# Kernel tuning notes

Hardware: AMD Instinct MI355X
Metric: run time of the kernel (lower is better)

Reference implementation:

```python
import jax, jax.numpy as jnp
import numpy as np

# dims: G groups, A authors/group, P posts/author, DIN token-pooled feat, DEMB sentence-BERT dim
G, A, P, DIN, DEMB, HP, HA = 16, 64, 32, 768, 384, 256, 128


def setup_inputs() -> dict:
    key = jax.random.key(0)
    ks = jax.random.split(key, 8)
    s = lambda k, shape, scale: (jax.random.normal(k, shape, jnp.float32) * scale)
    return {
        "x": jax.random.normal(ks[0], (G, A, P, DIN), jnp.float32),
        "w_embed": s(ks[1], (DIN, DEMB), 0.02),   # BERT pooled-projection stand-in
        "b_embed": jnp.zeros((DEMB,), jnp.float32),
        "k_post": s(ks[2], (DEMB, 4 * HP), 0.05),  # Keras LSTM kernel, gates [i|f|c|o]
        "r_post": s(ks[3], (HP, 4 * HP), 0.05),    # recurrent kernel
        "b_post": jnp.zeros((4 * HP,), jnp.float32),
        "k_auth": s(ks[4], (HP, 4 * HA), 0.05),
        "r_auth": s(ks[5], (HA, 4 * HA), 0.05),
        "b_auth": jnp.zeros((4 * HA,), jnp.float32),
    }


def _lstm(x, Wk, Wr, b):
    """Keras-style LSTM, returns final hidden state. x: [B,T,D] -> [B,H]."""
    B = x.shape[0]
    H = Wr.shape[0]
    # precompute input projections for all timesteps in one GEMM: [T,B,4H]
    z = jnp.einsum('btd,dh->tbh', x, Wk) + b

    def step(carry, zt):
        h, c = carry
        g = zt + h @ Wr
        i, f, gg, o = jnp.split(g, 4, axis=-1)  # Keras gate order i,f,c,o
        c = jax.nn.sigmoid(f) * c + jax.nn.sigmoid(i) * jnp.tanh(gg)
        h = jax.nn.sigmoid(o) * jnp.tanh(c)
        return (h, c), None

    h0 = jnp.zeros((B, H), x.dtype)
    (h, _), _ = jax.lax.scan(step, (h0, h0), z)
    return h


def reference(x, w_embed, b_embed, k_post, r_post, b_post, k_auth, r_auth, b_auth):
    g, a, p, _ = x.shape
    # sentence embedding per post (BERT stand-in): [G,A,P,DEMB]
    e = jnp.einsum('gapd,de->gape', x, w_embed) + b_embed
    # LSTM over posts, batched across all (group, author) pairs: [G,A,HP]
    h_post = _lstm(e.reshape(g * a, p, e.shape[-1]), k_post, r_post, b_post)
    h_post = h_post.reshape(g, a, -1)
    # LSTM over authors: [G,HA]
    return _lstm(h_post, k_auth, r_auth, b_auth)
```

## Files before the change

kernel.cpp:

```cpp
#include <hip/hip_runtime.h>
#include <cstdint>
#include <cstddef>

#define G_    16
#define A_    64
#define P_    32
#define DIN_  768
#define DEMB_ 384
#define HP_   256
#define HA_   128
#define GA_   1024
#define N1_   1024
#define N2_   512
#define TCH   16

typedef float    f32x4   __attribute__((ext_vector_type(4)));
typedef _Float16 half8_t __attribute__((ext_vector_type(8)));
typedef _Float16 half4_t __attribute__((ext_vector_type(4)));

__device__ __forceinline__ float sigmoidf_(float x) { return 1.0f / (1.0f + __expf(-x)); }
__device__ __forceinline__ float tanhf_(float x) { return 2.0f / (1.0f + __expf(-2.0f * x)) - 1.0f; }
__device__ __forceinline__ _Float16 us2h(unsigned short u) { _Float16 h; __builtin_memcpy(&h, &u, 2); return h; }
__device__ __forceinline__ unsigned short h2us(_Float16 h) { unsigned short u; __builtin_memcpy(&u, &h, 2); return u; }


__global__ __launch_bounds__(256) void k_wk(const float* __restrict__ w_embed,
                                            const float* __restrict__ k_post,
                                            float* __restrict__ Bmat) {
    int j  = blockIdx.x * 256 + threadIdx.x;
    int k0 = blockIdx.y * 4;
    float acc0 = 0.f, acc1 = 0.f, acc2 = 0.f, acc3 = 0.f;
    for (int d = 0; d < DEMB_; ++d) {
        float kp = k_post[(size_t)d * N1_ + j];
        acc0 += w_embed[(size_t)(k0 + 0) * DEMB_ + d] * kp;
        acc1 += w_embed[(size_t)(k0 + 1) * DEMB_ + d] * kp;
        acc2 += w_embed[(size_t)(k0 + 2) * DEMB_ + d] * kp;
        acc3 += w_embed[(size_t)(k0 + 3) * DEMB_ + d] * kp;
    }
    Bmat[(size_t)(k0 + 0) * N1_ + j] = acc0;
    Bmat[(size_t)(k0 + 1) * N1_ + j] = acc1;
    Bmat[(size_t)(k0 + 2) * N1_ + j] = acc2;
    Bmat[(size_t)(k0 + 3) * N1_ + j] = acc3;
}

__global__ __launch_bounds__(256) void k_bias_p(const float* __restrict__ b_embed,
                                                const float* __restrict__ k_post,
                                                const float* __restrict__ b_post,
                                                float* __restrict__ biasZp) {
    int p = blockIdx.x * 256 + threadIdx.x;
    int n = (p >> 6) * 16 + (p & 15) + 256 * ((p >> 4) & 3);
    float acc = b_post[n];
    for (int d = 0; d < DEMB_; ++d)
        acc += b_embed[d] * k_post[(size_t)d * N1_ + n];
    biasZp[p] = acc;
}

__global__ __launch_bounds__(256) void k_t16(const float* __restrict__ Bmat,
                                             _Float16* __restrict__ Bt16) {
    __shared__ float tile[64][65];
    const int tid = threadIdx.x;
    const int p0 = blockIdx.x * 64;
    const int k0 = blockIdx.y * 64;
    const int jgrp = p0 >> 6;
#pragma unroll
    for (int i = 0; i < 16; ++i) {
        int idx = i * 256 + tid;
        int pp = idx & 63, kk = idx >> 6;
        int n = jgrp * 16 + (pp & 15) + 256 * ((pp >> 4) & 3);
        tile[pp][kk] = Bmat[(size_t)(k0 + kk) * N1_ + n];
    }
    __syncthreads();
    const int pp = tid >> 2;
    const int kq = (tid & 3) * 16;
    _Float16 buf[16];
#pragma unroll
    for (int i = 0; i < 16; ++i) buf[i] = (_Float16)tile[pp][kq + i];
    _Float16* dst = &Bt16[(size_t)(p0 + pp) * DIN_ + k0 + kq];
    *(half8_t*)dst       = *(half8_t*)&buf[0];
    *(half8_t*)(dst + 8) = *(half8_t*)&buf[8];
}

__global__ __launch_bounds__(256) void k_bfrag(const float* __restrict__ r_post,
                                               _Float16* __restrict__ Bfrag) {
    int idx = blockIdx.x * 256 + threadIdx.x;
    int pt = idx >> 9;
    int kt = (idx >> 6) & 7;
    int l  = idx & 63;
    int p = pt * 16 + (l & 15);
    int n = (p >> 6) * 16 + (p & 15) + 256 * ((p >> 4) & 3);
    int kb = kt * 32 + (l >> 4) * 8;
    _Float16 buf[8];
#pragma unroll
    for (int s = 0; s < 8; ++s) buf[s] = (_Float16)r_post[(size_t)(kb + s) * N1_ + n];
    *(half8_t*)&Bfrag[(size_t)idx * 8] = *(half8_t*)buf;
}

#define ZBM 128
#define ZBN 256
#define ZBK 32
#define ZPAD 40

__global__ __launch_bounds__(512, 2) void k_zgemm(const float* __restrict__ x,
                                                  const _Float16* __restrict__ Bt16,
                                                  const float* __restrict__ biasZp,
                                                  _Float16* __restrict__ Zq, int tbase) {
    __shared__ union {
        struct { _Float16 As[ZBM][ZPAD], Bs[ZBN][ZPAD]; } S;
        _Float16 Hs[64][264];
    } u;

    const int bid = blockIdx.x;
    const int wg  = (bid & 7) * 64 + (bid >> 3);
    const int bm  = (wg & 127) * ZBM;
    const int bn  = (wg >> 7) * ZBN;
    const int tid = threadIdx.x;

    const int arow = tid >> 2, akq = (tid & 3) * 8;
    const int brow = tid >> 1, bkq = (tid & 1) * 16;
    const int lane = tid & 63, w = tid >> 6;
    const int wm = (w >> 2) * 64, wn = (w & 3) * 64;
    const int frc = lane & 15, frk = (lane >> 4) * 8;

    const int crow = bm + arow;
    const size_t xrow = (size_t)(crow >> 4) * P_ + tbase + (crow & 15);
    const float*    aptr = &x[xrow * DIN_ + akq];
    const _Float16* bptr = &Bt16[(size_t)(bn + brow) * DIN_ + bkq];

    f32x4 acc[4][4];
#pragma unroll
    for (int i = 0; i < 4; ++i)
#pragma unroll
        for (int j = 0; j < 4; ++j) acc[i][j] = (f32x4)0.0f;

    float4 a0 = *(const float4*)aptr;
    float4 a1 = *(const float4*)(aptr + 4);
    uint4  b0 = *(const uint4*)bptr;
    uint4  b1 = *(const uint4*)(bptr + 8);

    const int NK = DIN_ / ZBK;
    for (int kt = 0; kt < NK; ++kt) {
        const int kn = (kt + 1 < NK) ? (kt + 1) * ZBK : kt * ZBK;
        float4 na0 = *(const float4*)(aptr + kn);
        float4 na1 = *(const float4*)(aptr + kn + 4);
        uint4  nb0 = *(const uint4*)(bptr + kn);
        uint4  nb1 = *(const uint4*)(bptr + kn + 8);

        half8_t ahv;
        {
            float av[8] = {a0.x,a0.y,a0.z,a0.w,a1.x,a1.y,a1.z,a1.w};
#pragma unroll
            for (int i = 0; i < 8; ++i) ahv[i] = (_Float16)av[i];
        }

        __syncthreads();
        *(half8_t*)&u.S.As[arow][akq]  = ahv;
        *(uint4*)&u.S.Bs[brow][bkq]     = b0;
        *(uint4*)&u.S.Bs[brow][bkq + 8] = b1;
        __syncthreads();

        half8_t bf[4];
#pragma unroll
        for (int fn = 0; fn < 4; ++fn)
            bf[fn] = *(const half8_t*)&u.S.Bs[wn + fn * 16 + frc][frk];
#pragma unroll
        for (int fm = 0; fm < 4; ++fm) {
            half8_t aH = *(const half8_t*)&u.S.As[wm + fm * 16 + frc][frk];
#pragma unroll
            for (int fn = 0; fn < 4; ++fn)
                acc[fm][fn] = __builtin_amdgcn_mfma_f32_16x16x32_f16(aH, bf[fn], acc[fm][fn], 0, 0, 0);
        }
        a0 = na0; a1 = na1; b0 = nb0; b1 = nb1;
    }

    float bzv[4];
#pragma unroll
    for (int fn = 0; fn < 4; ++fn) bzv[fn] = biasZp[bn + wn + fn * 16 + frc];

#pragma unroll
    for (int half_ = 0; half_ < 2; ++half_) {
        __syncthreads();
        if ((w >> 2) == half_) {
#pragma unroll
            for (int fm = 0; fm < 4; ++fm)
#pragma unroll
                for (int fn = 0; fn < 4; ++fn)
#pragma unroll
                    for (int r = 0; r < 4; ++r) {
                        int rl = fm * 16 + (lane >> 4) * 4 + r;
                        int cl = wn + fn * 16 + frc;
                        int clp = ((cl >> 6) * 16 + (cl & 15)) * 4 + ((cl >> 4) & 3);
                        u.Hs[rl][clp] = (_Float16)(acc[fm][fn][r] + bzv[fn]);
                    }
        }
        __syncthreads();
#pragma unroll
        for (int i = 0; i < 4; ++i) {
            int id = i * 512 + tid;
            int r = id >> 5, cc = (id & 31) * 8;
            *(uint4*)&Zq[(size_t)(bm + half_ * 64 + r) * N1_ + bn + cc] = *(const uint4*)&u.Hs[r][cc];
        }
    }
}

__global__ __launch_bounds__(1024, 4) void k_rec(const _Float16* __restrict__ Zq,
                                                 const _Float16* __restrict__ Bfrag,
                                                 float* __restrict__ csave,
                                                 unsigned short* __restrict__ hsave,
                                                 float* __restrict__ hF32, int tbase) {
    __shared__ __align__(16) _Float16 wlds[16 * 8 * 64 * 8];
    __shared__ __align__(16) _Float16 hbuf[2][4096];

    const int tid = threadIdx.x, lane = tid & 63, wv = tid >> 6;
    const int hl = lane & 15, l4 = lane >> 4;
    const int r0 = blockIdx.x * 16;
    const int hc = wv * 16 + hl;

    half8_t wreg[16];
#pragma unroll
    for (int q = 0; q < 2; ++q)
#pragma unroll
        for (int kt = 0; kt < 8; ++kt)
            wreg[q * 8 + kt] = *(const half8_t*)&Bfrag[(((size_t)(4 * wv + q) * 8 + kt) * 64 + lane) * 8];
#pragma unroll
    for (int kt = 0; kt < 8; ++kt)
        *(half8_t*)&wlds[((wv * 8 + kt) * 64 + lane) * 8] =
            *(const half8_t*)&Bfrag[(((size_t)(4 * wv + 2) * 8 + kt) * 64 + lane) * 8];
    const _Float16* w3base = &Bfrag[((size_t)(4 * wv + 3) * 8 * 64 + lane) * 8];

    float cst[4];
    if (tbase == 0) {
#pragma unroll
        for (int i = 0; i < 4; ++i) cst[i] = 0.f;
    } else {
        f32x4 cv = *(const f32x4*)&csave[((size_t)blockIdx.x * 1024 + tid) * 4];
#pragma unroll
        for (int i = 0; i < 4; ++i) cst[i] = cv[i];
#pragma unroll
        for (int rr = 0; rr < 4; ++rr) {
            int row = l4 * 4 + rr;
            int lidx = (((hc >> 5) * 64) + (((hc & 31) >> 3) * 16 + row)) * 8 + (hc & 7);
            hbuf[0][lidx] = us2h(hsave[((size_t)(r0 + row)) * HP_ + hc]);
        }
    }
    __syncthreads();

    for (int tt = 0; tt < TCH; ++tt) {
        const int t = tbase + tt;
        const int cur = t & 1, nxt = cur ^ 1;

        half4_t zv[4];
#pragma unroll
        for (int rr = 0; rr < 4; ++rr)
            zv[rr] = *(const half4_t*)&Zq[((size_t)(r0 + l4 * 4 + rr) * TCH + tt) * N1_ + (size_t)hc * 4];

        f32x4 acc[4];
#pragma unroll
        for (int i = 0; i < 4; ++i) acc[i] = (f32x4)0.0f;

        if (t > 0) {
#pragma unroll
            for (int kt = 0; kt < 8; ++kt) {
                half8_t ah = *(const half8_t*)&hbuf[cur][(kt * 64 + lane) * 8];
                half8_t w3 = *(const half8_t*)&w3base[(size_t)kt * 512];
                half8_t b2 = *(const half8_t*)&wlds[((wv * 8 + kt) * 64 + lane) * 8];
                acc[0] = __builtin_amdgcn_mfma_f32_16x16x32_f16(ah, wreg[kt],     acc[0], 0, 0, 0);
                acc[1] = __builtin_amdgcn_mfma_f32_16x16x32_f16(ah, wreg[8 + kt], acc[1], 0, 0, 0);
                acc[2] = __builtin_amdgcn_mfma_f32_16x16x32_f16(ah, b2,           acc[2], 0, 0, 0);
                acc[3] = __builtin_amdgcn_mfma_f32_16x16x32_f16(ah, w3,           acc[3], 0, 0, 0);
            }
        }

        const bool last = (t == P_ - 1);
        const bool save = (tbase == 0) && (tt == TCH - 1);
#pragma unroll
        for (int rr = 0; rr < 4; ++rr) {
            float gi = acc[0][rr] + (float)zv[rr][0];
            float gf = acc[1][rr] + (float)zv[rr][1];
            float gg = acc[2][rr] + (float)zv[rr][2];
            float go = acc[3][rr] + (float)zv[rr][3];
            float cn = sigmoidf_(gf) * cst[rr] + sigmoidf_(gi) * tanhf_(gg);
            cst[rr] = cn;
            float hv = sigmoidf_(go) * tanhf_(cn);
            int row = l4 * 4 + rr;
            int lidx = (((hc >> 5) * 64) + (((hc & 31) >> 3) * 16 + row)) * 8 + (hc & 7);
            _Float16 hh = (_Float16)hv;
            hbuf[nxt][lidx] = hh;
            if (save) hsave[((size_t)(r0 + row)) * HP_ + hc] = h2us(hh);
            if (last) hF32[(size_t)(r0 + row) * HP_ + hc] = hv;
        }
        __syncthreads();
    }

    if (tbase == 0) {
        f32x4 cv;
#pragma unroll
        for (int i = 0; i < 4; ++i) cv[i] = cst[i];
        *(f32x4*)&csave[((size_t)blockIdx.x * 1024 + tid) * 4] = cv;
    }
}

__global__ __launch_bounds__(256) void k_zauth(const float* __restrict__ h,
                                               const float* __restrict__ k_auth,
                                               const float* __restrict__ b_auth,
                                               float* __restrict__ z_auth) {
    const int j = blockIdx.x * 256 + threadIdx.x;
    const int r0 = blockIdx.y * 4;
    float acc0 = b_auth[j], acc1 = acc0, acc2 = acc0, acc3 = acc0;
    for (int k = 0; k < HP_; ++k) {
        const float kp = k_auth[(size_t)k * N2_ + j];
        acc0 += h[(size_t)(r0 + 0) * HP_ + k] * kp;
        acc1 += h[(size_t)(r0 + 1) * HP_ + k] * kp;
        acc2 += h[(size_t)(r0 + 2) * HP_ + k] * kp;
        acc3 += h[(size_t)(r0 + 3) * HP_ + k] * kp;
    }
#pragma unroll
    for (int r = 0; r < 4; ++r) {
        const int b = r0 + r;
        const int g = b >> 6, a = b & 63;
        const float v = (r == 0) ? acc0 : (r == 1) ? acc1 : (r == 2) ? acc2 : acc3;
        z_auth[((size_t)a * G_ + g) * N2_ + j] = v;
    }
}

__global__ __launch_bounds__(1024) void k_author(const float* __restrict__ z_auth,
                                                 const float* __restrict__ r_auth,
                                                 float* __restrict__ out) {
    const int g = blockIdx.x;
    const int tid = threadIdx.x;
    const int j = tid >> 1;
    const int kh = tid & 1;

    __shared__ float hs[HA_];
    __shared__ float gs[N2_];

    float rc[64];
#pragma unroll
    for (int kk = 0; kk < 64; ++kk)
        rc[kk] = r_auth[(size_t)(kh * 64 + kk) * N2_ + j];

    float cj = 0.f;
    if (tid < HA_) hs[tid] = 0.f;
    __syncthreads();

    for (int a = 0; a < A_; ++a) {
        float acc = kh ? 0.f : z_auth[((size_t)a * G_ + g) * N2_ + j];
#pragma unroll
        for (int kk = 0; kk < 64; ++kk)
            acc += hs[kh * 64 + kk] * rc[kk];
        acc += __shfl_xor(acc, 1);
        if (!kh) gs[j] = acc;
        __syncthreads();
        if (tid < HA_) {
            const float i_ = sigmoidf_(gs[tid]);
            const float f_ = sigmoidf_(gs[tid + 128]);
            const float gg = gs[tid + 256];
            const float o_ = sigmoidf_(gs[tid + 384]);
            cj = f_ * cj + i_ * tanhf_(gg);
            hs[tid] = o_ * tanhf_(cj);
        }
        __syncthreads();
    }
    if (tid < HA_) out[(size_t)g * HA_ + tid] = hs[tid];
}

extern "C" void kernel_launch(void* const* d_in, const int* in_sizes, int n_in,
                              void* d_out, int out_size, void* d_ws, size_t ws_size,
                              hipStream_t stream) {
    const float* x       = (const float*)d_in[0];
    const float* w_embed = (const float*)d_in[1];
    const float* b_embed = (const float*)d_in[2];
    const float* k_post  = (const float*)d_in[3];
    const float* r_post  = (const float*)d_in[4];
    const float* b_post  = (const float*)d_in[5];
    const float* k_auth  = (const float*)d_in[6];
    const float* r_auth  = (const float*)d_in[7];
    const float* b_auth  = (const float*)d_in[8];
    float* out = (float*)d_out;

    char* wsb = (char*)d_ws;
    _Float16*       Zq     = (_Float16*)(wsb);
    float*          Bmat   = (float*)(wsb + (32ull << 20));
    _Float16*       Bt16   = (_Float16*)(wsb + (36ull << 20));
    _Float16*       Bfrag  = (_Float16*)(wsb + (38ull << 20));
    float*          biasZp = (float*)(wsb + (38ull << 20) + (512ull << 10));
    float*          csave  = (float*)(wsb + (39ull << 20));
    unsigned short* hsave  = (unsigned short*)(wsb + (40ull << 20));
    float*          hF32   = (float*)(wsb + (41ull << 20));
    float*          z_auth = (float*)(wsb + (42ull << 20));

    k_wk    <<<dim3(N1_ / 256, DIN_ / 4), 256, 0, stream>>>(w_embed, k_post, Bmat);
    k_bias_p<<<dim3(N1_ / 256), 256, 0, stream>>>(b_embed, k_post, b_post, biasZp);
    k_t16   <<<dim3(16, 12), 256, 0, stream>>>(Bmat, Bt16);
    k_bfrag <<<dim3(128), 256, 0, stream>>>(r_post, Bfrag);

    for (int ch = 0; ch < 2; ++ch) {
        k_zgemm<<<dim3(512), 512, 0, stream>>>(x, Bt16, biasZp, Zq, ch * TCH);
        k_rec  <<<dim3(64), 1024, 0, stream>>>(Zq, Bfrag, csave, hsave, hF32, ch * TCH);
    }

    k_zauth <<<dim3(N2_ / 256, GA_ / 4), 256, 0, stream>>>(hF32, k_auth, b_auth, z_auth);
    k_author<<<dim3(G_), 1024, 0, stream>>>(z_auth, r_auth, out);
}
```

Before: 414.3 us.

## Store Zq in recurrence-thread-major layout, prefetch gates, restructure author LSTM

The GEMM epilogue now writes Zq so each recurrent-kernel thread's 4 rows x 4 gates sit in one contiguous 32-byte chunk per timestep. The recurrence can then load its gate inputs with two 16-byte loads and prefetch the next timestep's values one step ahead, which hides global latency on the serial critical path. The author LSTM kernel moves to 512 threads, each holding a full 128-weight column in registers, reading hidden state as float4 and prefetching the next z. This removes the cross-lane shuffle but raises register pressure.

```diff
diff --git a/kernel.cpp b/kernel.cpp
--- a/kernel.cpp
+++ b/kernel.cpp
@@ -193,11 +193,25 @@
                     }
         }
         __syncthreads();
-#pragma unroll
-        for (int i = 0; i < 4; ++i) {
-            int id = i * 512 + tid;
-            int r = id >> 5, cc = (id & 31) * 8;
-            *(uint4*)&Zq[(size_t)(bm + half_ * 64 + r) * N1_ + bn + cc] = *(const uint4*)&u.Hs[r][cc];
+        const int brb = (bm + half_ * 64) >> 4;
+        const int rg  = brb >> 4;
+        const int l4r = (brb & 15) >> 2;
+#pragma unroll
+        for (int it = 0; it < 2; ++it) {
+            int unit = it * 512 + tid;
+            int tloc = unit >> 6, hcl = unit & 63;
+            _Float16 buf[16];
+#pragma unroll
+            for (int rr = 0; rr < 4; ++rr) {
+                half4_t h4 = *(const half4_t*)&u.Hs[tloc + 16 * rr][hcl * 4];
+                buf[rr * 4 + 0] = h4[0]; buf[rr * 4 + 1] = h4[1];
+                buf[rr * 4 + 2] = h4[2]; buf[rr * 4 + 3] = h4[3];
+            }
+            int wvg  = (bn >> 6) + (hcl >> 4);
+            int tid2 = wvg * 64 + l4r * 16 + (hcl & 15);
+            _Float16* dst = &Zq[((size_t)(tloc * 64 + rg) * 1024 + tid2) * 16];
+            *(uint4*)dst       = *(const uint4*)&buf[0];
+            *(uint4*)(dst + 8) = *(const uint4*)&buf[8];
         }
     }
 }
@@ -244,14 +258,20 @@
     }
     __syncthreads();
 
+    const _Float16* zp0 = &Zq[((size_t)blockIdx.x * 1024 + tid) * 16];
+    half8_t z01N = *(const half8_t*)zp0;
+    half8_t z23N = *(const half8_t*)(zp0 + 8);
+
     for (int tt = 0; tt < TCH; ++tt) {
         const int t = tbase + tt;
         const int cur = t & 1, nxt = cur ^ 1;
 
-        half4_t zv[4];
-#pragma unroll
-        for (int rr = 0; rr < 4; ++rr)
-            zv[rr] = *(const half4_t*)&Zq[((size_t)(r0 + l4 * 4 + rr) * TCH + tt) * N1_ + (size_t)hc * 4];
+        half8_t z01 = z01N, z23 = z23N;
+        if (tt + 1 < TCH) {
+            const _Float16* zpn = zp0 + (size_t)(tt + 1) * 1048576;
+            z01N = *(const half8_t*)zpn;
+            z23N = *(const half8_t*)(zpn + 8);
+        }
 
         f32x4 acc[4];
 #pragma unroll
@@ -261,8 +281,8 @@
 #pragma unroll
             for (int kt = 0; kt < 8; ++kt) {
                 half8_t ah = *(const half8_t*)&hbuf[cur][(kt * 64 + lane) * 8];
+                half8_t b2 = *(const half8_t*)&wlds[((wv * 8 + kt) * 64 + lane) * 8];
                 half8_t w3 = *(const half8_t*)&w3base[(size_t)kt * 512];
-                half8_t b2 = *(const half8_t*)&wlds[((wv * 8 + kt) * 64 + lane) * 8];
                 acc[0] = __builtin_amdgcn_mfma_f32_16x16x32_f16(ah, wreg[kt],     acc[0], 0, 0, 0);
                 acc[1] = __builtin_amdgcn_mfma_f32_16x16x32_f16(ah, wreg[8 + kt], acc[1], 0, 0, 0);
                 acc[2] = __builtin_amdgcn_mfma_f32_16x16x32_f16(ah, b2,           acc[2], 0, 0, 0);
@@ -274,10 +294,12 @@
         const bool save = (tbase == 0) && (tt == TCH - 1);
 #pragma unroll
         for (int rr = 0; rr < 4; ++rr) {
-            float gi = acc[0][rr] + (float)zv[rr][0];
-            float gf = acc[1][rr] + (float)zv[rr][1];
-            float gg = acc[2][rr] + (float)zv[rr][2];
-            float go = acc[3][rr] + (float)zv[rr][3];
+            const half8_t zsrc = (rr < 2) ? z01 : z23;
+            const int o = (rr & 1) * 4;
+            float gi = acc[0][rr] + (float)zsrc[o + 0];
+            float gf = acc[1][rr] + (float)zsrc[o + 1];
+            float gg = acc[2][rr] + (float)zsrc[o + 2];
+            float go = acc[3][rr] + (float)zsrc[o + 3];
             float cn = sigmoidf_(gf) * cst[rr] + sigmoidf_(gi) * tanhf_(gg);
             cst[rr] = cn;
             float hv = sigmoidf_(go) * tanhf_(cn);
@@ -322,33 +344,37 @@
     }
 }
 
-__global__ __launch_bounds__(1024) void k_author(const float* __restrict__ z_auth,
-                                                 const float* __restrict__ r_auth,
-                                                 float* __restrict__ out) {
+__global__ __launch_bounds__(512, 2) void k_author(const float* __restrict__ z_auth,
+                                                   const float* __restrict__ r_auth,
+                                                   float* __restrict__ out) {
     const int g = blockIdx.x;
     const int tid = threadIdx.x;
-    const int j = tid >> 1;
-    const int kh = tid & 1;
 
     __shared__ float hs[HA_];
     __shared__ float gs[N2_];
 
-    float rc[64];
-#pragma unroll
-    for (int kk = 0; kk < 64; ++kk)
-        rc[kk] = r_auth[(size_t)(kh * 64 + kk) * N2_ + j];
+    float rc[HA_];
+#pragma unroll
+    for (int k = 0; k < HA_; ++k)
+        rc[k] = r_auth[(size_t)k * N2_ + tid];
 
     float cj = 0.f;
     if (tid < HA_) hs[tid] = 0.f;
     __syncthreads();
 
+    float zn = z_auth[(size_t)g * N2_ + tid];
     for (int a = 0; a < A_; ++a) {
-        float acc = kh ? 0.f : z_auth[((size_t)a * G_ + g) * N2_ + j];
-#pragma unroll
-        for (int kk = 0; kk < 64; ++kk)
-            acc += hs[kh * 64 + kk] * rc[kk];
-        acc += __shfl_xor(acc, 1);
-        if (!kh) gs[j] = acc;
+        float acc0 = zn, acc1 = 0.f, acc2 = 0.f, acc3 = 0.f;
+        if (a + 1 < A_) zn = z_auth[((size_t)(a + 1) * G_ + g) * N2_ + tid];
+#pragma unroll
+        for (int k = 0; k < HA_; k += 4) {
+            float4 h4 = *(const float4*)&hs[k];
+            acc0 += h4.x * rc[k];
+            acc1 += h4.y * rc[k + 1];
+            acc2 += h4.z * rc[k + 2];
+            acc3 += h4.w * rc[k + 3];
+        }
+        gs[tid] = (acc0 + acc1) + (acc2 + acc3);
         __syncthreads();
         if (tid < HA_) {
             const float i_ = sigmoidf_(gs[tid]);
@@ -399,5 +425,5 @@
     }
 
     k_zauth <<<dim3(N2_ / 256, GA_ / 4), 256, 0, stream>>>(hF32, k_auth, b_auth, z_auth);
-    k_author<<<dim3(G_), 1024, 0, stream>>>(z_auth, r_auth, out);
-}
+    k_author<<<dim3(G_), 512, 0, stream>>>(z_auth, r_auth, out);
+}
```

After: 406.3 us, median of 3. Within noise of the previous version (-1.9%).
